# Performance work log

Hardware: AMD Instinct MI355X
Metric: run time of the kernel (lower is better)

Reference implementation:

```python
import jax, jax.numpy as jnp
import numpy as np

R, MAXI, MAXO = 333, 119, 12   # n ROIs, max roi input size, max roi reduced size
E, H = 3328, 8                  # embed dim (concat 3325 + pad 3), heads
HD = E // H                     # 416
CONCAT = 3325
EPS = 1e-5


def _roi_layout():
    """Deterministic synthetic ROI sizes + gather maps for vectorized ragged encode."""
    sizes = 30 + (7 * np.arange(R)) % 90            # per-ROI input widths
    reduced = 8 + np.arange(R) % 5                  # per-ROI output widths
    reduced[332] = 8                                # makes concat+3 divisible by 8
    starts = np.concatenate([[0], np.cumsum(sizes)[:-1]])
    total = int(sizes.sum())                        # 24696
    in_idx = np.minimum(starts[:, None] + np.arange(MAXI)[None, :], total - 1)
    in_mask = (np.arange(MAXI)[None, :] < sizes[:, None]).astype(np.float32)
    out_idx = np.concatenate([i * MAXO + np.arange(reduced[i]) for i in range(R)])
    assert out_idx.shape[0] == CONCAT
    return jnp.asarray(in_idx), jnp.asarray(in_mask), jnp.asarray(out_idx)


def _bn(x, g, b):
    # training-mode BatchNorm1d: biased batch stats (matches torch normalization)
    m = x.mean(0)
    v = x.var(0)
    return (x - m) * jax.lax.rsqrt(v + EPS) * g + b


def _lrelu(x, s):
    return jnp.where(x > 0, x, s * x)


def setup_inputs() -> dict:
    key = jax.random.key(0)
    ks = jax.random.split(key, 16)
    B, TOTAL = 2048, 24696
    f32 = jnp.float32
    return {
        'x': jax.random.normal(ks[0], (B, TOTAL), f32),
        'enc_W': jax.random.normal(ks[1], (R, MAXO, MAXI), f32) * 0.1,
        'enc_b': jax.random.normal(ks[2], (R, MAXO), f32) * 0.02,
        'bn1_g': jnp.ones((CONCAT,), f32),
        'bn1_b': jnp.zeros((CONCAT,), f32),
        'Wqkv': jax.random.normal(ks[3], (3 * E, E), f32) * (1.0 / np.sqrt(E)),
        'bqkv': jnp.zeros((3 * E,), f32),
        'Wo': jax.random.normal(ks[4], (E, E), f32) * (1.0 / np.sqrt(E)),
        'bo': jnp.zeros((E,), f32),
        'W1': jax.random.normal(ks[5], (1024, E), f32) * (1.0 / np.sqrt(E)),
        'b1': jnp.zeros((1024,), f32),
        'bn2_g': jnp.ones((1024,), f32),
        'bn2_b': jnp.zeros((1024,), f32),
        'W2': jax.random.normal(ks[6], (300, 1024), f32) * (1.0 / 32.0),
        'b2': jnp.zeros((300,), f32),
        'Wc': jax.random.normal(ks[7], (180, 300), f32) * 0.06,
        'bc': jnp.zeros((180,), f32),
    }


def reference(x, enc_W, enc_b, bn1_g, bn1_b, Wqkv, bqkv, Wo, bo,
              W1, b1, bn2_g, bn2_b, W2, b2, Wc, bc):
    in_idx, in_mask, out_idx = _roi_layout()
    B = x.shape[0]
    # --- vectorized ragged per-ROI Linear (replaces 333-way python loop) ---
    xp = x[:, in_idx] * in_mask                     # [B, R, MAXI], padded slices
    y = jnp.einsum('bri,roi->bro', xp, enc_W) + enc_b  # [B, R, MAXO]
    y = y.reshape(B, R * MAXO)[:, out_idx]          # ragged concat -> [B, 3325]
    # per-ROI BN+LeakyReLU(0.3) == per-feature on the concat
    y = _lrelu(_bn(y, bn1_g, bn1_b), 0.3)
    y = jnp.pad(y, ((0, 0), (1, 2)))                # F.pad (1, 2) -> [B, 3328]
    # --- MultiheadAttention, seq_len = 1 (input unsqueezed to [1, B, E]) ---
    qkv = y @ Wqkv.T + bqkv                         # [B, 3E]
    q, k, v = jnp.split(qkv, 3, axis=-1)
    q = q.reshape(B, H, 1, HD)
    k = k.reshape(B, H, 1, HD)
    v = v.reshape(B, H, 1, HD)
    s = jnp.einsum('bhqd,bhkd->bhqk', q, k) / jnp.sqrt(jnp.float32(HD))
    a = jax.nn.softmax(s, axis=-1)                  # trivially 1 for L=1, kept faithful
    o = jnp.einsum('bhqk,bhkd->bhqd', a, v).reshape(B, E)
    o = o @ Wo.T + bo
    r = _lrelu(_bn(o @ W1.T + b1, bn2_g, bn2_b), 0.1)
    reg_out = r @ W2.T + b2                         # [B, 300]
    y_pred = jax.nn.softmax(reg_out @ Wc.T + bc, axis=-1)  # [B, 180]
    return reg_out, y_pred
```

## Files before the change

kernel.cpp:

```cpp
#include <hip/hip_runtime.h>
#include <hip/hip_bf16.h>

#define B_      2048
#define R_      333
#define MAXI_   119
#define MAXO_   12
#define CONCAT_ 3325
#define E_      3328
#define TOTAL_  24696
#define HID_    1024
#define NREG_   300
#define NCLS_   180
#define EPS_    1e-5f
#define NSLOT_  128
#define PSTR_   3328
#define NS2_    128

typedef __attribute__((ext_vector_type(8))) short bf16x8;
typedef __attribute__((ext_vector_type(4))) float f32x4;

static __device__ inline unsigned short f2bf_rne(float f) {
  unsigned u;
  __builtin_memcpy(&u, &f, 4);
  u += 0x7fff + ((u >> 16) & 1);
  return (unsigned short)(u >> 16);
}
static __device__ inline float bf2f(unsigned short s) {
  unsigned u = (unsigned)s << 16;
  float f;
  __builtin_memcpy(&f, &u, 4);
  return f;
}

__global__ void layout_kernel(int* __restrict__ starts, int* __restrict__ red_starts) {
  if (threadIdx.x == 0 && blockIdx.x == 0) {
    int s = 0, rs = 0;
    for (int r = 0; r < R_; ++r) {
      starts[r] = s;
      red_starts[r] = rs;
      s += 30 + (7 * r) % 90;
      rs += (r == 332) ? 8 : (8 + r % 5);
    }
  }
}

__device__ __forceinline__ void rowdot_body(
    const float* __restrict__ A, const float* __restrict__ v, const float* __restrict__ b,
    float* __restrict__ out, int N, int K, int jb) {
  int wid = threadIdx.x >> 6, lane = threadIdx.x & 63;
  int j = jb * 4 + wid;
  if (j >= N) return;
  const float* row = A + (size_t)j * K;
  float s = 0.f;
  for (int k = lane; k < K; k += 64) s = fmaf(row[k], v[k], s);
  for (int o = 32; o; o >>= 1) s += __shfl_down(s, o);
  if (lane == 0) out[j] = s + b[j];
}

__device__ __forceinline__ void pack_w_body(const float* __restrict__ enc_W,
                                            const int* __restrict__ starts,
                                            unsigned short* __restrict__ Wpk, int r) {
  int tid = threadIdx.x;
  int kc = tid >> 6, lane = tid & 63;
  int size = 30 + (7 * r) % 90;
  int s8 = starts[r] & 7;
  int oc = lane & 15;
  int k0 = kc * 32 + (lane >> 4) * 8;
  unsigned short o[8];
#pragma unroll
  for (int e = 0; e < 8; ++e) {
    int k = k0 + e - s8;
    float v = 0.f;
    if (oc < MAXO_ && k >= 0 && k < size) v = enc_W[((size_t)r * MAXO_ + oc) * MAXI_ + k];
    o[e] = f2bf_rne(v);
  }
  unsigned short* dst = Wpk + ((size_t)r * 4 + kc) * 512 + lane * 8;
  *(ushort4*)dst = *(ushort4*)&o[0];
  *(ushort4*)(dst + 4) = *(ushort4*)&o[4];
}

#define NTR_   ((E_ / 64) * (E_ / 64))
#define NC4A_  (HID_ * E_ / 4)
#define NC4B_  (NREG_ * HID_ / 4)
#define NCAST_ ((NC4A_ + NC4B_ + 255) / 256)
__global__ __launch_bounds__(256) void prep_kernel(
    const float* __restrict__ Wo, const float* __restrict__ Wv,
    unsigned short* __restrict__ WoT, unsigned short* __restrict__ WvT,
    const float* __restrict__ W1, unsigned short* __restrict__ W1b,
    const float* __restrict__ W2, unsigned short* __restrict__ W2b,
    const float* __restrict__ bv, const float* __restrict__ bo, float* __restrict__ t1v,
    const float* __restrict__ enc_W, const int* __restrict__ starts,
    unsigned short* __restrict__ Wpk) {
  __shared__ float tile[64][65];
  int bid = blockIdx.x;
  if (bid < 2 * NTR_) {
    int z = bid / NTR_, rem = bid % NTR_;
    const float* in = z ? Wv : Wo;
    unsigned short* out = z ? WvT : WoT;
    int c0 = (rem % 52) * 64, r0 = (rem / 52) * 64;
    int t = threadIdx.x;
    int ci = t & 63, ri0 = t >> 6;
    for (int ri = ri0; ri < 64; ri += 4)
      tile[ri][ci] = in[(size_t)(r0 + ri) * E_ + c0 + ci];
    __syncthreads();
    int rj = t & 63, i0 = t >> 6;
    for (int i = i0; i < 64; i += 4)
      out[(size_t)(c0 + i) * E_ + r0 + rj] = f2bf_rne(tile[rj][i]);
  } else if (bid < 2 * NTR_ + NCAST_) {
    int i = (bid - 2 * NTR_) * 256 + threadIdx.x;
    const float* src; unsigned short* dst; int idx;
    if (i < NC4A_) { src = W1; dst = W1b; idx = i; }
    else if (i < NC4A_ + NC4B_) { src = W2; dst = W2b; idx = i - NC4A_; }
    else return;
    float4 v = ((const float4*)src)[idx];
    ushort4 o;
    o.x = f2bf_rne(v.x); o.y = f2bf_rne(v.y); o.z = f2bf_rne(v.z); o.w = f2bf_rne(v.w);
    ((ushort4*)dst)[idx] = o;
  } else if (bid < 2 * NTR_ + NCAST_ + E_ / 4) {
    rowdot_body(Wo, bv, bo, t1v, E_, E_, bid - 2 * NTR_ - NCAST_);
  } else {
    pack_w_body(enc_W, starts, Wpk, bid - 2 * NTR_ - NCAST_ - E_ / 4);
  }
}

__device__ __forceinline__ void encode_body(
    const float* __restrict__ x, const unsigned short* __restrict__ Wpk,
    const float* __restrict__ enc_b, const int* __restrict__ starts,
    const int* __restrict__ red_starts,
    unsigned short* __restrict__ yT, float* __restrict__ pS1, float* __restrict__ pS2,
    int r, int bg) {
  int tid = threadIdx.x;
  int wid = tid >> 6, lane = tid & 63;
  int lr = lane & 15, kg = lane >> 4;

  int size = 30 + (7 * r) % 90;
  int red  = (r == 332) ? 8 : (8 + r % 5);
  int st   = starts[r];
  int s8   = st & 7;
  int a0   = st & ~7;
  int rs   = red_starts[r];
  int nkc  = (s8 + size + 31) >> 5;
  int kmax = TOTAL_ - a0;

  bf16x8 wf[4];
  const unsigned short* wp = Wpk + (size_t)r * 2048 + lane * 8;
#pragma unroll
  for (int kc = 0; kc < 4; ++kc) wf[kc] = *(const bf16x8*)(wp + kc * 512);

  float bofs[4];
#pragma unroll
  for (int reg = 0; reg < 4; ++reg) {
    int oc = kg * 4 + reg;
    bofs[reg] = (oc < MAXO_) ? enc_b[r * MAXO_ + oc] : 0.f;
  }

  int ks[4];
#pragma unroll
  for (int kc = 0; kc < 4; ++kc) {
    int k0 = kc * 32 + kg * 8;
    if (k0 + 8 > kmax) k0 = kmax - 8;
    ks[kc] = k0;
  }

  for (int tp = 0; tp < 2; ++tp) {
    int b0a = bg * 256 + wid * 64 + tp * 32;
    int b0b = b0a + 16;
    const float* xra = x + (size_t)(b0a + lr) * TOTAL_ + a0;
    const float* xrb = x + (size_t)(b0b + lr) * TOTAL_ + a0;
    float4 va[4][2], vb[4][2];
#pragma unroll
    for (int kc = 0; kc < 4; ++kc) {
      if (kc < nkc) {
        va[kc][0] = *(const float4*)(xra + ks[kc]);
        va[kc][1] = *(const float4*)(xra + ks[kc] + 4);
        vb[kc][0] = *(const float4*)(xrb + ks[kc]);
        vb[kc][1] = *(const float4*)(xrb + ks[kc] + 4);
      }
    }
    f32x4 acca = {0.f, 0.f, 0.f, 0.f}, accb = {0.f, 0.f, 0.f, 0.f};
#pragma unroll
    for (int kc = 0; kc < 4; ++kc) {
      if (kc < nkc) {
        bf16x8 xfa, xfb;
#pragma unroll
        for (int e = 0; e < 4; ++e) {
          xfa[e]     = (short)f2bf_rne(va[kc][0][e]);
          xfa[e + 4] = (short)f2bf_rne(va[kc][1][e]);
          xfb[e]     = (short)f2bf_rne(vb[kc][0][e]);
          xfb[e + 4] = (short)f2bf_rne(vb[kc][1][e]);
        }
        acca = __builtin_amdgcn_mfma_f32_16x16x32_bf16(wf[kc], xfa, acca, 0, 0, 0);
        accb = __builtin_amdgcn_mfma_f32_16x16x32_bf16(wf[kc], xfb, accb, 0, 0, 0);
      }
    }
#pragma unroll
    for (int half = 0; half < 2; ++half) {
      int b0 = half ? b0b : b0a;
      f32x4 acc = half ? accb : acca;
      int slot = b0 >> 4;
#pragma unroll
      for (int reg = 0; reg < 4; ++reg) {
        int oc = kg * 4 + reg;
        if (oc < red) {
          float v = acc[reg] + bofs[reg];
          yT[(size_t)(rs + oc) * B_ + b0 + lr] = f2bf_rne(v);
          float a = v, s2 = v * v;
#pragma unroll
          for (int m = 1; m <= 8; m <<= 1) { a += __shfl_xor(a, m); s2 += __shfl_xor(s2, m); }
          if (lr == 0) {
            pS1[slot * PSTR_ + rs + oc] = a;
            pS2[slot * PSTR_ + rs + oc] = s2;
          }
        }
      }
    }
  }
}

template <int KS, bool OUT_BF16>
__device__ __forceinline__ void gemm_body(
    const unsigned short* __restrict__ A, const unsigned short* __restrict__ W,
    float* __restrict__ Cf, unsigned short* __restrict__ Cb,
    int M, int N, int K, int bx, int by, int bz, unsigned short* smem) {
  unsigned short* a_lds = smem;
  unsigned short* b_lds = smem + 8192;
  int tid = threadIdx.x;
  int wid = tid >> 6, lane = tid & 63;
  int wr = wid >> 1, wc = wid & 1;
  int row0 = by * 128, col0 = bx * 128;
  int lr = lane & 15, kg = lane >> 4;
  int Klocal = K / KS;
  int kbase = bz * Klocal;

  int srow = tid >> 2, sk = (tid & 3) * 8;
  const unsigned short* aptr0 = A + (size_t)(row0 + srow) * K + kbase + sk;
  const unsigned short* aptr1 = aptr0 + (size_t)64 * K;
  int bcol0 = col0 + srow;      if (bcol0 > N - 1) bcol0 = N - 1;
  int bcol1 = col0 + 64 + srow; if (bcol1 > N - 1) bcol1 = N - 1;
  const unsigned short* bptr0 = W + (size_t)bcol0 * K + kbase + sk;
  const unsigned short* bptr1 = W + (size_t)bcol1 * K + kbase + sk;

  f32x4 acc[4][4] = {};
  int nk = Klocal >> 5;

#define STAGE_(buf, kc)                                                                             \
  do {                                                                                              \
    __builtin_amdgcn_global_load_lds((const __attribute__((address_space(1))) void*)(aptr0 + (kc)), \
        (__attribute__((address_space(3))) void*)(a_lds + (buf) * 4096 + wid * 512), 16, 0, 0);     \
    __builtin_amdgcn_global_load_lds((const __attribute__((address_space(1))) void*)(aptr1 + (kc)), \
        (__attribute__((address_space(3))) void*)(a_lds + (buf) * 4096 + 2048 + wid * 512), 16, 0, 0); \
    __builtin_amdgcn_global_load_lds((const __attribute__((address_space(1))) void*)(bptr0 + (kc)), \
        (__attribute__((address_space(3))) void*)(b_lds + (buf) * 4096 + wid * 512), 16, 0, 0);     \
    __builtin_amdgcn_global_load_lds((const __attribute__((address_space(1))) void*)(bptr1 + (kc)), \
        (__attribute__((address_space(3))) void*)(b_lds + (buf) * 4096 + 2048 + wid * 512), 16, 0, 0); \
  } while (0)

  STAGE_(0, 0);
  __syncthreads();
  int cur = 0;
  for (int t = 0; t < nk; ++t) {
    if (t + 1 < nk) STAGE_(cur ^ 1, (t + 1) * 32);
    bf16x8 a[4], b[4];
#pragma unroll
    for (int f = 0; f < 4; ++f) {
      a[f] = *(const bf16x8*)(a_lds + cur * 4096 + (wr * 64 + f * 16 + lr) * 32 + kg * 8);
      b[f] = *(const bf16x8*)(b_lds + cur * 4096 + (wc * 64 + f * 16 + lr) * 32 + kg * 8);
    }
#pragma unroll
    for (int i = 0; i < 4; ++i)
#pragma unroll
      for (int j = 0; j < 4; ++j)
        acc[i][j] = __builtin_amdgcn_mfma_f32_16x16x32_bf16(a[i], b[j], acc[i][j], 0, 0, 0);
    __syncthreads();
    cur ^= 1;
  }
#undef STAGE_

#pragma unroll
  for (int j = 0; j < 4; ++j) {
    int ccol = col0 + wc * 64 + j * 16 + lr;
    if (ccol >= N) continue;
#pragma unroll
    for (int i = 0; i < 4; ++i) {
#pragma unroll
      for (int reg = 0; reg < 4; ++reg) {
        int crow = row0 + wr * 64 + i * 16 + kg * 4 + reg;
        float v = acc[i][j][reg];
        if (KS == 1) {
          if (OUT_BF16) Cb[(size_t)crow * N + ccol] = f2bf_rne(v);
          else          Cf[(size_t)crow * N + ccol] = v;
        } else {
          Cf[((size_t)bz * M + crow) * N + ccol] = v;
        }
      }
    }
  }
}

#define WA_NB_  ((E_ / 128) * (HID_ / 128))
#define ENC_NB_ (R_ * 8)
__global__ __launch_bounds__(256) void enc_wa_kernel(
    const float* __restrict__ x, const unsigned short* __restrict__ Wpk,
    const float* __restrict__ enc_b, const int* __restrict__ starts,
    const int* __restrict__ red_starts,
    unsigned short* __restrict__ yT, float* __restrict__ pS1, float* __restrict__ pS2,
    const unsigned short* __restrict__ W1b, const unsigned short* __restrict__ WoT,
    unsigned short* __restrict__ Wa_bf,
    const float* __restrict__ W1, const float* __restrict__ t1v,
    const float* __restrict__ b1, float* __restrict__ zbv) {
  __shared__ __align__(16) unsigned short smem[16384];
  int bid = blockIdx.x;
  if (bid < WA_NB_) {
    gemm_body<1, true>(W1b, WoT, nullptr, Wa_bf, HID_, E_, E_,
                       bid % (E_ / 128), bid / (E_ / 128), 0, smem);
  } else if (bid < WA_NB_ + ENC_NB_) {
    int eb = bid - WA_NB_;
    encode_body(x, Wpk, enc_b, starts, red_starts, yT, pS1, pS2, eb >> 3, eb & 7);
  } else {
    rowdot_body(W1, t1v, b1, zbv, HID_, E_, bid - WA_NB_ - ENC_NB_);
  }
}

__global__ __launch_bounds__(256) void bn1_stats_kernel(const float* __restrict__ pS1,
                                                        const float* __restrict__ pS2,
                                                        float* __restrict__ mean, float* __restrict__ rstd) {
  int c = blockIdx.x * 256 + threadIdx.x;
  if (c >= CONCAT_) return;
  float s = 0.f, s2 = 0.f;
  for (int i = 0; i < NSLOT_; ++i) { s += pS1[i * PSTR_ + c]; s2 += pS2[i * PSTR_ + c]; }
  float m = s / B_;
  float v = s2 / B_ - m * m;
  mean[c] = m;
  rstd[c] = rsqrtf(v + EPS_);
}

#define WB_NB_ ((E_ / 128) * (HID_ / 128) * 2)
#define TR_NB_ ((E_ / 64) * (B_ / 64))
__global__ __launch_bounds__(256) void trans_wb_kernel(
    const unsigned short* __restrict__ yT, const float* __restrict__ mean,
    const float* __restrict__ rstd, const float* __restrict__ g,
    const float* __restrict__ bb, unsigned short* __restrict__ Y,
    const unsigned short* __restrict__ Wa_bf, const unsigned short* __restrict__ WvT,
    float* __restrict__ Cpart) {
  __shared__ __align__(16) unsigned short smem[16384];
  int bid = blockIdx.x;
  if (bid < WB_NB_) {
    int z = bid / (WB_NB_ / 2), rem = bid % (WB_NB_ / 2);
    gemm_body<2, false>(Wa_bf, WvT, Cpart, nullptr, HID_, E_, E_,
                        rem % (E_ / 128), rem / (E_ / 128), z, smem);
  } else {
    int tb = bid - WB_NB_;
    int cc0 = (tb % 52) * 64, b0 = (tb / 52) * 64;
    float (*tile)[65] = (float(*)[65])smem;
    int t = threadIdx.x;
    int bi = t & 63, ci0 = t >> 6;
    for (int ci = ci0; ci < 64; ci += 4) {
      int c = cc0 + ci - 1;
      float v = 0.f;
      if (c >= 0 && c < CONCAT_) {
        float f = bf2f(yT[(size_t)c * B_ + b0 + bi]);
        v = (f - mean[c]) * rstd[c] * g[c] + bb[c];
        v = v > 0.f ? v : 0.3f * v;
      }
      tile[ci][bi] = v;
    }
    __syncthreads();
    int cj = t & 63, bj0 = t >> 6;
    for (int bj = bj0; bj < 64; bj += 4)
      Y[(size_t)(b0 + bj) * E_ + cc0 + cj] = f2bf_rne(tile[cj][bj]);
  }
}

__global__ __launch_bounds__(256) void combine_wb_kernel(const float* __restrict__ part,
                                                         unsigned short* __restrict__ out) {
  const int MN = HID_ * E_;
  int i = blockIdx.x * 256 + threadIdx.x;
  if (i >= MN) return;
  out[i] = f2bf_rne(part[i] + part[(size_t)MN + i]);
}

template <int KS, bool OUT_BF16>
__global__ __launch_bounds__(256) void gemm_kernel(
    const unsigned short* __restrict__ A, const unsigned short* __restrict__ W,
    float* __restrict__ Cf, unsigned short* __restrict__ Cb, int M, int N, int K) {
  __shared__ __align__(16) unsigned short smem[16384];
  gemm_body<KS, OUT_BF16>(A, W, Cf, Cb, M, N, K, blockIdx.x, blockIdx.y, blockIdx.z, smem);
}

__global__ __launch_bounds__(256) void combZ_stats_kernel(
    const float* __restrict__ Cpart, const float* __restrict__ zb,
    float* __restrict__ Z, float* __restrict__ pS, float* __restrict__ pS2) {
  int c = blockIdx.x * 256 + threadIdx.x;
  int ry = blockIdx.y;
  float zbc = zb[c];
  float s1 = 0.f, s2 = 0.f;
  for (int r = ry * 16; r < ry * 16 + 16; ++r) {
    float v = zbc;
#pragma unroll
    for (int z = 0; z < 4; ++z) v += Cpart[((size_t)z * B_ + r) * HID_ + c];
    Z[(size_t)r * HID_ + c] = v;
    s1 += v; s2 = fmaf(v, v, s2);
  }
  pS[ry * HID_ + c] = s1;
  pS2[ry * HID_ + c] = s2;
}

__global__ __launch_bounds__(256) void colstats_final_kernel(
    const float* __restrict__ pS, const float* __restrict__ pS2,
    float* __restrict__ mean, float* __restrict__ rstd) {
  int c = blockIdx.x * 256 + threadIdx.x;
  if (c >= HID_) return;
  float s = 0.f, s2 = 0.f;
  for (int i = 0; i < NS2_; ++i) { s += pS[i * HID_ + c]; s2 += pS2[i * HID_ + c]; }
  float m = s / B_;
  float v = s2 / B_ - m * m;
  mean[c] = m;
  rstd[c] = rsqrtf(v + EPS_);
}

__global__ __launch_bounds__(256) void bn2_apply_kernel(
    const float* __restrict__ Z, const float* __restrict__ mean, const float* __restrict__ rstd,
    const float* __restrict__ g, const float* __restrict__ bb, unsigned short* __restrict__ R) {
  int i = blockIdx.x * 256 + threadIdx.x;
  int c = i & (HID_ - 1);
  float v = (Z[i] - mean[c]) * rstd[c] * g[c] + bb[c];
  v = v > 0.f ? v : 0.1f * v;
  R[i] = f2bf_rne(v);
}

__global__ __launch_bounds__(256) void classifier_kernel(
    const float* __restrict__ Cpart, const float* __restrict__ b2,
    const float* __restrict__ Wc, const float* __restrict__ bc,
    float* __restrict__ reg_out, float* __restrict__ ypred) {
  int b = blockIdx.x;
  __shared__ __align__(16) float rrow[NREG_];
  __shared__ float sl[256];
  int tid = threadIdx.x;
  for (int i = tid; i < NREG_; i += 256) {
    float s = b2[i];
#pragma unroll
    for (int z = 0; z < 4; ++z) s += Cpart[((size_t)z * B_ + b) * NREG_ + i];
    rrow[i] = s;
    reg_out[(size_t)b * NREG_ + i] = s;
  }
  __syncthreads();
  float s = -1e30f;
  if (tid < NCLS_) {
    const float* w = Wc + (size_t)tid * NREG_;
    float acc = 0.f;
    for (int k = 0; k < NREG_; k += 4) {
      float4 wv = *(const float4*)(w + k);
      float4 rv = *(const float4*)(&rrow[k]);
      acc = fmaf(wv.x, rv.x, acc); acc = fmaf(wv.y, rv.y, acc);
      acc = fmaf(wv.z, rv.z, acc); acc = fmaf(wv.w, rv.w, acc);
    }
    s = acc + bc[tid];
  }
  sl[tid] = s;
  __syncthreads();
  for (int o = 128; o > 0; o >>= 1) {
    if (tid < o) sl[tid] = fmaxf(sl[tid], sl[tid + o]);
    __syncthreads();
  }
  float mx = sl[0];
  __syncthreads();
  float e = (tid < NCLS_) ? __expf(s - mx) : 0.f;
  sl[tid] = e;
  __syncthreads();
  for (int o = 128; o > 0; o >>= 1) {
    if (tid < o) sl[tid] += sl[tid + o];
    __syncthreads();
  }
  if (tid < NCLS_) ypred[(size_t)b * NCLS_ + tid] = e / sl[0];
}

extern "C" void kernel_launch(void* const* d_in, const int* in_sizes, int n_in,
                              void* d_out, int out_size, void* d_ws, size_t ws_size,
                              hipStream_t stream) {
  const float* x     = (const float*)d_in[0];
  const float* enc_W = (const float*)d_in[1];
  const float* enc_b = (const float*)d_in[2];
  const float* bn1_g = (const float*)d_in[3];
  const float* bn1_b = (const float*)d_in[4];
  const float* Wqkv  = (const float*)d_in[5];
  const float* bqkv  = (const float*)d_in[6];
  const float* Wo    = (const float*)d_in[7];
  const float* bo    = (const float*)d_in[8];
  const float* W1    = (const float*)d_in[9];
  const float* b1    = (const float*)d_in[10];
  const float* bn2_g = (const float*)d_in[11];
  const float* bn2_b = (const float*)d_in[12];
  const float* W2    = (const float*)d_in[13];
  const float* b2    = (const float*)d_in[14];
  const float* Wc    = (const float*)d_in[15];
  const float* bc    = (const float*)d_in[16];

  char* ws = (char*)d_ws;
  size_t off = 0;
  auto alloc = [&](size_t bytes) -> void* {
    void* p = ws + off;
    off += (bytes + 255) & ~(size_t)255;
    return p;
  };

  unsigned short* yT     = (unsigned short*)alloc((size_t)CONCAT_ * B_ * 2);
  float*          pS1b   = (float*)alloc((size_t)NSLOT_ * PSTR_ * 4);
  float*          pS2b   = (float*)alloc((size_t)NSLOT_ * PSTR_ * 4);
  float*          mean1  = (float*)alloc(CONCAT_ * 4);
  float*          rstd1  = (float*)alloc(CONCAT_ * 4);
  unsigned short* Ybf    = (unsigned short*)alloc((size_t)B_ * E_ * 2);
  unsigned short* Rbf    = (unsigned short*)alloc((size_t)B_ * HID_ * 2);
  unsigned short* WoT_bf = (unsigned short*)alloc((size_t)E_ * E_ * 2);
  unsigned short* WvT_bf = (unsigned short*)alloc((size_t)E_ * E_ * 2);
  unsigned short* W1_bf  = (unsigned short*)alloc((size_t)HID_ * E_ * 2);
  unsigned short* W2_bf  = (unsigned short*)alloc((size_t)NREG_ * HID_ * 2);
  unsigned short* Wa_bf  = (unsigned short*)alloc((size_t)HID_ * E_ * 2);
  unsigned short* Wb_bf  = (unsigned short*)alloc((size_t)HID_ * E_ * 2);
  unsigned short* Wpk    = (unsigned short*)alloc((size_t)R_ * 2048 * 2);
  float*          Cpart  = (float*)alloc((size_t)4 * B_ * HID_ * 4);
  float*          t1v    = (float*)alloc(E_ * 4);
  float*          zbv    = (float*)alloc(HID_ * 4);
  float*          partS  = (float*)alloc((size_t)NS2_ * HID_ * 4);
  float*          partS2 = (float*)alloc((size_t)NS2_ * HID_ * 4);
  float*          mean2  = (float*)alloc(HID_ * 4);
  float*          rstd2  = (float*)alloc(HID_ * 4);
  int*            starts = (int*)alloc(R_ * 4);
  int*            redst  = (int*)alloc(R_ * 4);

  float* Z = (float*)yT;

  layout_kernel<<<1, 1, 0, stream>>>(starts, redst);
  prep_kernel<<<2 * NTR_ + NCAST_ + E_ / 4 + R_, 256, 0, stream>>>(
      Wo, Wqkv + (size_t)2 * E_ * E_, WoT_bf, WvT_bf,
      W1, W1_bf, W2, W2_bf, bqkv + 2 * E_, bo, t1v, enc_W, starts, Wpk);
  enc_wa_kernel<<<WA_NB_ + ENC_NB_ + HID_ / 4, 256, 0, stream>>>(
      x, Wpk, enc_b, starts, redst, yT, pS1b, pS2b, W1_bf, WoT_bf, Wa_bf, W1, t1v, b1, zbv);
  bn1_stats_kernel<<<(CONCAT_ + 255) / 256, 256, 0, stream>>>(pS1b, pS2b, mean1, rstd1);
  trans_wb_kernel<<<WB_NB_ + TR_NB_, 256, 0, stream>>>(
      yT, mean1, rstd1, bn1_g, bn1_b, Ybf, Wa_bf, WvT_bf, Cpart);
  combine_wb_kernel<<<(HID_ * E_ + 255) / 256, 256, 0, stream>>>(Cpart, Wb_bf);
  gemm_kernel<4, false><<<dim3(HID_ / 128, B_ / 128, 4), 256, 0, stream>>>(
      Ybf, Wb_bf, Cpart, nullptr, B_, HID_, E_);
  combZ_stats_kernel<<<dim3(HID_ / 256, NS2_), 256, 0, stream>>>(Cpart, zbv, Z, partS, partS2);
  colstats_final_kernel<<<(HID_ + 255) / 256, 256, 0, stream>>>(partS, partS2, mean2, rstd2);
  bn2_apply_kernel<<<(B_ * HID_) / 256, 256, 0, stream>>>(Z, mean2, rstd2, bn2_g, bn2_b, Rbf);
  gemm_kernel<4, false><<<dim3((NREG_ + 127) / 128, B_ / 128, 4), 256, 0, stream>>>(
      Rbf, W2_bf, Cpart, nullptr, B_, NREG_, HID_);
  float* reg_out = (float*)d_out;
  classifier_kernel<<<B_, 256, 0, stream>>>(
      Cpart, b2, Wc, bc, reg_out, reg_out + (size_t)B_ * NREG_);
}
```

Before: 336.9 us.

## Regroup prep, encode and weight-fold kernels; drop split-K combine and stats launch

Reorganizes the kernel schedule. The enc_W packing and the first rowdot move into a small leading kernel. The encoder then runs alongside the weight transposes and casts in one grand kernel. BN1 stats are merged into the Wa GEMM launch, and the Wb GEMM switches from split-K with a separate combine kernel to a single pass with bf16 output. The encoder inner loop is also simplified from two paired tiles with preloaded registers to one 16-row tile per step, which lowers register pressure but gives less memory-level parallelism. The aim is fewer launches and better overlap between independent stages, at the cost of fewer blocks for the Wb GEMM.

```diff
diff --git a/kernel.cpp b/kernel.cpp
--- a/kernel.cpp
+++ b/kernel.cpp
@@ -79,22 +79,107 @@
   *(ushort4*)(dst + 4) = *(ushort4*)&o[4];
 }
 
-#define NTR_   ((E_ / 64) * (E_ / 64))
-#define NC4A_  (HID_ * E_ / 4)
-#define NC4B_  (NREG_ * HID_ / 4)
-#define NCAST_ ((NC4A_ + NC4B_ + 255) / 256)
-__global__ __launch_bounds__(256) void prep_kernel(
+__global__ __launch_bounds__(256) void packw_rd1_kernel(
+    const float* __restrict__ enc_W, const int* __restrict__ starts,
+    unsigned short* __restrict__ Wpk,
+    const float* __restrict__ Wo, const float* __restrict__ bv,
+    const float* __restrict__ bo, float* __restrict__ t1v) {
+  int bid = blockIdx.x;
+  if (bid < R_) pack_w_body(enc_W, starts, Wpk, bid);
+  else          rowdot_body(Wo, bv, bo, t1v, E_, E_, bid - R_);
+}
+
+__device__ __forceinline__ void encode_body(
+    const float* __restrict__ x, const unsigned short* __restrict__ Wpk,
+    const float* __restrict__ enc_b, const int* __restrict__ starts,
+    const int* __restrict__ red_starts,
+    unsigned short* __restrict__ yT, float* __restrict__ pS1, float* __restrict__ pS2,
+    int r, int bg) {
+  int tid = threadIdx.x;
+  int wid = tid >> 6, lane = tid & 63;
+  int lr = lane & 15, kg = lane >> 4;
+
+  int size = 30 + (7 * r) % 90;
+  int red  = (r == 332) ? 8 : (8 + r % 5);
+  int st   = starts[r];
+  int s8   = st & 7;
+  int a0   = st & ~7;
+  int rs   = red_starts[r];
+  int nkc  = (s8 + size + 31) >> 5;
+  int kmax = TOTAL_ - a0;
+
+  bf16x8 wf[4];
+  const unsigned short* wp = Wpk + (size_t)r * 2048 + lane * 8;
+#pragma unroll
+  for (int kc = 0; kc < 4; ++kc) wf[kc] = *(const bf16x8*)(wp + kc * 512);
+
+  float bofs[4];
+#pragma unroll
+  for (int reg = 0; reg < 4; ++reg) {
+    int oc = kg * 4 + reg;
+    bofs[reg] = (oc < MAXO_) ? enc_b[r * MAXO_ + oc] : 0.f;
+  }
+
+  for (int t = 0; t < 4; ++t) {
+    int b0 = bg * 256 + wid * 64 + t * 16;
+    const float* xrow = x + (size_t)(b0 + lr) * TOTAL_ + a0;
+    f32x4 acc = {0.f, 0.f, 0.f, 0.f};
+#pragma unroll
+    for (int kc = 0; kc < 4; ++kc) {
+      if (kc < nkc) {
+        int k0 = kc * 32 + kg * 8;
+        if (k0 + 8 > kmax) k0 = kmax - 8;
+        float4 v0 = *(const float4*)(xrow + k0);
+        float4 v1 = *(const float4*)(xrow + k0 + 4);
+        bf16x8 xf;
+        xf[0] = (short)f2bf_rne(v0.x); xf[1] = (short)f2bf_rne(v0.y);
+        xf[2] = (short)f2bf_rne(v0.z); xf[3] = (short)f2bf_rne(v0.w);
+        xf[4] = (short)f2bf_rne(v1.x); xf[5] = (short)f2bf_rne(v1.y);
+        xf[6] = (short)f2bf_rne(v1.z); xf[7] = (short)f2bf_rne(v1.w);
+        acc = __builtin_amdgcn_mfma_f32_16x16x32_bf16(wf[kc], xf, acc, 0, 0, 0);
+      }
+    }
+    int slot = b0 >> 4;
+#pragma unroll
+    for (int reg = 0; reg < 4; ++reg) {
+      int oc = kg * 4 + reg;
+      if (oc < red) {
+        float v = acc[reg] + bofs[reg];
+        yT[(size_t)(rs + oc) * B_ + b0 + lr] = f2bf_rne(v);
+        float a = v, s2 = v * v;
+#pragma unroll
+        for (int m = 1; m <= 8; m <<= 1) { a += __shfl_xor(a, m); s2 += __shfl_xor(s2, m); }
+        if (lr == 0) {
+          pS1[slot * PSTR_ + rs + oc] = a;
+          pS2[slot * PSTR_ + rs + oc] = s2;
+        }
+      }
+    }
+  }
+}
+
+#define ENC_NB_ (R_ * 8)
+#define NTR_    ((E_ / 64) * (E_ / 64))
+#define NC4A_   (HID_ * E_ / 4)
+#define NC4B_   (NREG_ * HID_ / 4)
+#define NCAST_  ((NC4A_ + NC4B_ + 255) / 256)
+__global__ __launch_bounds__(256) void grand_kernel(
+    const float* __restrict__ x, const unsigned short* __restrict__ Wpk,
+    const float* __restrict__ enc_b, const int* __restrict__ starts,
+    const int* __restrict__ red_starts,
+    unsigned short* __restrict__ yT, float* __restrict__ pS1, float* __restrict__ pS2,
     const float* __restrict__ Wo, const float* __restrict__ Wv,
     unsigned short* __restrict__ WoT, unsigned short* __restrict__ WvT,
     const float* __restrict__ W1, unsigned short* __restrict__ W1b,
     const float* __restrict__ W2, unsigned short* __restrict__ W2b,
-    const float* __restrict__ bv, const float* __restrict__ bo, float* __restrict__ t1v,
-    const float* __restrict__ enc_W, const int* __restrict__ starts,
-    unsigned short* __restrict__ Wpk) {
+    const float* __restrict__ t1v, const float* __restrict__ b1, float* __restrict__ zbv) {
   __shared__ float tile[64][65];
   int bid = blockIdx.x;
-  if (bid < 2 * NTR_) {
-    int z = bid / NTR_, rem = bid % NTR_;
+  if (bid < ENC_NB_) {
+    encode_body(x, Wpk, enc_b, starts, red_starts, yT, pS1, pS2, bid >> 3, bid & 7);
+  } else if (bid < ENC_NB_ + 2 * NTR_) {
+    int tb = bid - ENC_NB_;
+    int z = tb / NTR_, rem = tb % NTR_;
     const float* in = z ? Wv : Wo;
     unsigned short* out = z ? WvT : WoT;
     int c0 = (rem % 52) * 64, r0 = (rem / 52) * 64;
@@ -106,8 +191,8 @@
     int rj = t & 63, i0 = t >> 6;
     for (int i = i0; i < 64; i += 4)
       out[(size_t)(c0 + i) * E_ + r0 + rj] = f2bf_rne(tile[rj][i]);
-  } else if (bid < 2 * NTR_ + NCAST_) {
-    int i = (bid - 2 * NTR_) * 256 + threadIdx.x;
+  } else if (bid < ENC_NB_ + 2 * NTR_ + NCAST_) {
+    int i = (bid - ENC_NB_ - 2 * NTR_) * 256 + threadIdx.x;
     const float* src; unsigned short* dst; int idx;
     if (i < NC4A_) { src = W1; dst = W1b; idx = i; }
     else if (i < NC4A_ + NC4B_) { src = W2; dst = W2b; idx = i - NC4A_; }
@@ -116,104 +201,8 @@
     ushort4 o;
     o.x = f2bf_rne(v.x); o.y = f2bf_rne(v.y); o.z = f2bf_rne(v.z); o.w = f2bf_rne(v.w);
     ((ushort4*)dst)[idx] = o;
-  } else if (bid < 2 * NTR_ + NCAST_ + E_ / 4) {
-    rowdot_body(Wo, bv, bo, t1v, E_, E_, bid - 2 * NTR_ - NCAST_);
   } else {
-    pack_w_body(enc_W, starts, Wpk, bid - 2 * NTR_ - NCAST_ - E_ / 4);
-  }
-}
-
-__device__ __forceinline__ void encode_body(
-    const float* __restrict__ x, const unsigned short* __restrict__ Wpk,
-    const float* __restrict__ enc_b, const int* __restrict__ starts,
-    const int* __restrict__ red_starts,
-    unsigned short* __restrict__ yT, float* __restrict__ pS1, float* __restrict__ pS2,
-    int r, int bg) {
-  int tid = threadIdx.x;
-  int wid = tid >> 6, lane = tid & 63;
-  int lr = lane & 15, kg = lane >> 4;
-
-  int size = 30 + (7 * r) % 90;
-  int red  = (r == 332) ? 8 : (8 + r % 5);
-  int st   = starts[r];
-  int s8   = st & 7;
-  int a0   = st & ~7;
-  int rs   = red_starts[r];
-  int nkc  = (s8 + size + 31) >> 5;
-  int kmax = TOTAL_ - a0;
-
-  bf16x8 wf[4];
-  const unsigned short* wp = Wpk + (size_t)r * 2048 + lane * 8;
-#pragma unroll
-  for (int kc = 0; kc < 4; ++kc) wf[kc] = *(const bf16x8*)(wp + kc * 512);
-
-  float bofs[4];
-#pragma unroll
-  for (int reg = 0; reg < 4; ++reg) {
-    int oc = kg * 4 + reg;
-    bofs[reg] = (oc < MAXO_) ? enc_b[r * MAXO_ + oc] : 0.f;
-  }
-
-  int ks[4];
-#pragma unroll
-  for (int kc = 0; kc < 4; ++kc) {
-    int k0 = kc * 32 + kg * 8;
-    if (k0 + 8 > kmax) k0 = kmax - 8;
-    ks[kc] = k0;
-  }
-
-  for (int tp = 0; tp < 2; ++tp) {
-    int b0a = bg * 256 + wid * 64 + tp * 32;
-    int b0b = b0a + 16;
-    const float* xra = x + (size_t)(b0a + lr) * TOTAL_ + a0;
-    const float* xrb = x + (size_t)(b0b + lr) * TOTAL_ + a0;
-    float4 va[4][2], vb[4][2];
-#pragma unroll
-    for (int kc = 0; kc < 4; ++kc) {
-      if (kc < nkc) {
-        va[kc][0] = *(const float4*)(xra + ks[kc]);
-        va[kc][1] = *(const float4*)(xra + ks[kc] + 4);
-        vb[kc][0] = *(const float4*)(xrb + ks[kc]);
-        vb[kc][1] = *(const float4*)(xrb + ks[kc] + 4);
-      }
-    }
-    f32x4 acca = {0.f, 0.f, 0.f, 0.f}, accb = {0.f, 0.f, 0.f, 0.f};
-#pragma unroll
-    for (int kc = 0; kc < 4; ++kc) {
-      if (kc < nkc) {
-        bf16x8 xfa, xfb;
-#pragma unroll
-        for (int e = 0; e < 4; ++e) {
-          xfa[e]     = (short)f2bf_rne(va[kc][0][e]);
-          xfa[e + 4] = (short)f2bf_rne(va[kc][1][e]);
-          xfb[e]     = (short)f2bf_rne(vb[kc][0][e]);
-          xfb[e + 4] = (short)f2bf_rne(vb[kc][1][e]);
-        }
-        acca = __builtin_amdgcn_mfma_f32_16x16x32_bf16(wf[kc], xfa, acca, 0, 0, 0);
-        accb = __builtin_amdgcn_mfma_f32_16x16x32_bf16(wf[kc], xfb, accb, 0, 0, 0);
-      }
-    }
-#pragma unroll
-    for (int half = 0; half < 2; ++half) {
-      int b0 = half ? b0b : b0a;
-      f32x4 acc = half ? accb : acca;
-      int slot = b0 >> 4;
-#pragma unroll
-      for (int reg = 0; reg < 4; ++reg) {
-        int oc = kg * 4 + reg;
-        if (oc < red) {
-          float v = acc[reg] + bofs[reg];
-          yT[(size_t)(rs + oc) * B_ + b0 + lr] = f2bf_rne(v);
-          float a = v, s2 = v * v;
-#pragma unroll
-          for (int m = 1; m <= 8; m <<= 1) { a += __shfl_xor(a, m); s2 += __shfl_xor(s2, m); }
-          if (lr == 0) {
-            pS1[slot * PSTR_ + rs + oc] = a;
-            pS2[slot * PSTR_ + rs + oc] = s2;
-          }
-        }
-      }
-    }
+    rowdot_body(W1, t1v, b1, zbv, HID_, E_, bid - ENC_NB_ - 2 * NTR_ - NCAST_);
   }
 }
 
@@ -297,59 +286,43 @@
   }
 }
 
-#define WA_NB_  ((E_ / 128) * (HID_ / 128))
-#define ENC_NB_ (R_ * 8)
-__global__ __launch_bounds__(256) void enc_wa_kernel(
-    const float* __restrict__ x, const unsigned short* __restrict__ Wpk,
-    const float* __restrict__ enc_b, const int* __restrict__ starts,
-    const int* __restrict__ red_starts,
-    unsigned short* __restrict__ yT, float* __restrict__ pS1, float* __restrict__ pS2,
+#define WA_NB_ ((E_ / 128) * (HID_ / 128))
+__global__ __launch_bounds__(256) void wa_stats_kernel(
     const unsigned short* __restrict__ W1b, const unsigned short* __restrict__ WoT,
     unsigned short* __restrict__ Wa_bf,
-    const float* __restrict__ W1, const float* __restrict__ t1v,
-    const float* __restrict__ b1, float* __restrict__ zbv) {
+    const float* __restrict__ pS1, const float* __restrict__ pS2,
+    float* __restrict__ mean, float* __restrict__ rstd) {
   __shared__ __align__(16) unsigned short smem[16384];
   int bid = blockIdx.x;
   if (bid < WA_NB_) {
     gemm_body<1, true>(W1b, WoT, nullptr, Wa_bf, HID_, E_, E_,
                        bid % (E_ / 128), bid / (E_ / 128), 0, smem);
-  } else if (bid < WA_NB_ + ENC_NB_) {
-    int eb = bid - WA_NB_;
-    encode_body(x, Wpk, enc_b, starts, red_starts, yT, pS1, pS2, eb >> 3, eb & 7);
   } else {
-    rowdot_body(W1, t1v, b1, zbv, HID_, E_, bid - WA_NB_ - ENC_NB_);
-  }
-}
-
-__global__ __launch_bounds__(256) void bn1_stats_kernel(const float* __restrict__ pS1,
-                                                        const float* __restrict__ pS2,
-                                                        float* __restrict__ mean, float* __restrict__ rstd) {
-  int c = blockIdx.x * 256 + threadIdx.x;
-  if (c >= CONCAT_) return;
-  float s = 0.f, s2 = 0.f;
-  for (int i = 0; i < NSLOT_; ++i) { s += pS1[i * PSTR_ + c]; s2 += pS2[i * PSTR_ + c]; }
-  float m = s / B_;
-  float v = s2 / B_ - m * m;
-  mean[c] = m;
-  rstd[c] = rsqrtf(v + EPS_);
-}
-
-#define WB_NB_ ((E_ / 128) * (HID_ / 128) * 2)
+    int c = (bid - WA_NB_) * 256 + threadIdx.x;
+    if (c >= CONCAT_) return;
+    float s = 0.f, s2 = 0.f;
+    for (int i = 0; i < NSLOT_; ++i) { s += pS1[i * PSTR_ + c]; s2 += pS2[i * PSTR_ + c]; }
+    float m = s / B_;
+    float v = s2 / B_ - m * m;
+    mean[c] = m;
+    rstd[c] = rsqrtf(v + EPS_);
+  }
+}
+
 #define TR_NB_ ((E_ / 64) * (B_ / 64))
 __global__ __launch_bounds__(256) void trans_wb_kernel(
     const unsigned short* __restrict__ yT, const float* __restrict__ mean,
     const float* __restrict__ rstd, const float* __restrict__ g,
     const float* __restrict__ bb, unsigned short* __restrict__ Y,
     const unsigned short* __restrict__ Wa_bf, const unsigned short* __restrict__ WvT,
-    float* __restrict__ Cpart) {
+    unsigned short* __restrict__ Wb_bf) {
   __shared__ __align__(16) unsigned short smem[16384];
   int bid = blockIdx.x;
-  if (bid < WB_NB_) {
-    int z = bid / (WB_NB_ / 2), rem = bid % (WB_NB_ / 2);
-    gemm_body<2, false>(Wa_bf, WvT, Cpart, nullptr, HID_, E_, E_,
-                        rem % (E_ / 128), rem / (E_ / 128), z, smem);
+  if (bid < WA_NB_) {
+    gemm_body<1, true>(Wa_bf, WvT, nullptr, Wb_bf, HID_, E_, E_,
+                       bid % (E_ / 128), bid / (E_ / 128), 0, smem);
   } else {
-    int tb = bid - WB_NB_;
+    int tb = bid - WA_NB_;
     int cc0 = (tb % 52) * 64, b0 = (tb / 52) * 64;
     float (*tile)[65] = (float(*)[65])smem;
     int t = threadIdx.x;
@@ -369,14 +342,6 @@
     for (int bj = bj0; bj < 64; bj += 4)
       Y[(size_t)(b0 + bj) * E_ + cc0 + cj] = f2bf_rne(tile[cj][bj]);
   }
-}
-
-__global__ __launch_bounds__(256) void combine_wb_kernel(const float* __restrict__ part,
-                                                         unsigned short* __restrict__ out) {
-  const int MN = HID_ * E_;
-  int i = blockIdx.x * 256 + threadIdx.x;
-  if (i >= MN) return;
-  out[i] = f2bf_rne(part[i] + part[(size_t)MN + i]);
 }
 
 template <int KS, bool OUT_BF16>
@@ -530,15 +495,16 @@
   float* Z = (float*)yT;
 
   layout_kernel<<<1, 1, 0, stream>>>(starts, redst);
-  prep_kernel<<<2 * NTR_ + NCAST_ + E_ / 4 + R_, 256, 0, stream>>>(
+  packw_rd1_kernel<<<R_ + E_ / 4, 256, 0, stream>>>(
+      enc_W, starts, Wpk, Wo, bqkv + 2 * E_, bo, t1v);
+  grand_kernel<<<ENC_NB_ + 2 * NTR_ + NCAST_ + HID_ / 4, 256, 0, stream>>>(
+      x, Wpk, enc_b, starts, redst, yT, pS1b, pS2b,
       Wo, Wqkv + (size_t)2 * E_ * E_, WoT_bf, WvT_bf,
-      W1, W1_bf, W2, W2_bf, bqkv + 2 * E_, bo, t1v, enc_W, starts, Wpk);
-  enc_wa_kernel<<<WA_NB_ + ENC_NB_ + HID_ / 4, 256, 0, stream>>>(
-      x, Wpk, enc_b, starts, redst, yT, pS1b, pS2b, W1_bf, WoT_bf, Wa_bf, W1, t1v, b1, zbv);
-  bn1_stats_kernel<<<(CONCAT_ + 255) / 256, 256, 0, stream>>>(pS1b, pS2b, mean1, rstd1);
-  trans_wb_kernel<<<WB_NB_ + TR_NB_, 256, 0, stream>>>(
-      yT, mean1, rstd1, bn1_g, bn1_b, Ybf, Wa_bf, WvT_bf, Cpart);
-  combine_wb_kernel<<<(HID_ * E_ + 255) / 256, 256, 0, stream>>>(Cpart, Wb_bf);
+      W1, W1_bf, W2, W2_bf, t1v, b1, zbv);
+  wa_stats_kernel<<<WA_NB_ + (CONCAT_ + 255) / 256, 256, 0, stream>>>(
+      W1_bf, WoT_bf, Wa_bf, pS1b, pS2b, mean1, rstd1);
+  trans_wb_kernel<<<WA_NB_ + TR_NB_, 256, 0, stream>>>(
+      yT, mean1, rstd1, bn1_g, bn1_b, Ybf, Wa_bf, WvT_bf, Wb_bf);
   gemm_kernel<4, false><<<dim3(HID_ / 128, B_ / 128, 4), 256, 0, stream>>>(
       Ybf, Wb_bf, Cpart, nullptr, B_, HID_, E_);
   combZ_stats_kernel<<<dim3(HID_ / 256, NS2_), 256, 0, stream>>>(Cpart, zbv, Z, partS, partS2);
```

Result: slower. 351.0 us (+4.2%).
